# Kernel tuning notes

Measured on AMD Instinct MI355X. Metric: run time of the kernel, lower is better.

## Reference

```python
import jax, jax.numpy as jnp
import numpy as np

B, L, D = 4, 2048, 2048
H, KVH, HD = 16, 4, 128          # num_heads, num_kv_heads, head_dim = D // H
M = 16                           # mem_tokens
BASE = 10000.0
EPS = 1.1920929e-07              # torch F.rms_norm default eps = fp32 machine eps


def _rms_norm(x):
    # normalize over last dim, no learned weight (matches F.rms_norm(x, (hd,)))
    return x * jax.lax.rsqrt(jnp.mean(x * x, axis=-1, keepdims=True) + EPS)


def _apply_rotary(x, cos, sin):
    # x: [B, h, T, HD]; cos/sin: [1, 1, T, HD//2]
    half = x.shape[-1] // 2
    x1, x2 = x[..., :half], x[..., half:]
    return jnp.concatenate([x1 * cos + x2 * sin, -x1 * sin + x2 * cos], axis=-1)


def setup_inputs() -> dict:
    key = jax.random.key(0)
    k0, k1, k2, k3, k4 = jax.random.split(key, 5)
    kv_dim = KVH * HD
    s = 0.02
    return {
        "x": jax.random.normal(k0, (B, L, D), dtype=jnp.float32),
        "Wq": jax.random.normal(k1, (D, D), dtype=jnp.float32) * s,
        "Wk": jax.random.normal(k2, (kv_dim, D), dtype=jnp.float32) * s,
        "Wv": jax.random.normal(k3, (kv_dim, D), dtype=jnp.float32) * s,
        "Wproj": jax.random.normal(k4, (D, D), dtype=jnp.float32) * s,
        "q_gain": jnp.full((H,), 1.0, dtype=jnp.float32),
    }


def reference(x, Wq, Wk, Wv, Wproj, q_gain):
    Bx, Lx, Dx = x.shape
    # QKV projections (Linear: x @ W.T), split into heads -> [B, h, L, HD]
    q = (x @ Wq.T).reshape(Bx, Lx, H, HD).transpose(0, 2, 1, 3)
    k = (x @ Wk.T).reshape(Bx, Lx, KVH, HD).transpose(0, 2, 1, 3)
    v = (x @ Wv.T).reshape(Bx, Lx, KVH, HD).transpose(0, 2, 1, 3)
    # QK RMSNorm
    q = _rms_norm(q)
    k = _rms_norm(k)
    # RoPE on the non-memory tokens only
    T = Lx - M
    inv_freq = 1.0 / BASE ** (jnp.arange(0, HD, 2, dtype=jnp.float32) / HD)
    freqs = jnp.outer(jnp.arange(T, dtype=jnp.float32), inv_freq)  # [T, HD//2]
    cos = jnp.cos(freqs)[None, None]
    sin = jnp.sin(freqs)[None, None]
    q = jnp.concatenate([q[:, :, :M], _apply_rotary(q[:, :, M:], cos, sin)], axis=2)
    k = jnp.concatenate([k[:, :, :M], _apply_rotary(k[:, :, M:], cos, sin)], axis=2)
    # per-head gain on q
    q = q * q_gain[None, :, None, None]
    # GQA attention: group q heads by kv head (matches repeat_interleave ordering)
    rep = H // KVH
    qg = q.reshape(Bx, KVH, rep, Lx, HD)
    scale = 1.0 / np.sqrt(HD).astype(np.float32)
    scores = jnp.einsum('bgrqd,bgkd->bgrqk', qg, k) * scale  # [B, KVH, rep, L, L]
    causal = jnp.tril(jnp.ones((Lx, Lx), dtype=bool))
    scores = jnp.where(causal, scores, -jnp.inf)
    p = jax.nn.softmax(scores, axis=-1)
    y = jnp.einsum('bgrqk,bgkd->bgrqd', p, v)                # [B, KVH, rep, L, HD]
    y = y.reshape(Bx, H, Lx, HD).transpose(0, 2, 1, 3).reshape(Bx, Lx, Dx)
    return y @ Wproj.T
```

## Files before the change

kernel.cpp:

```cpp
#include <hip/hip_runtime.h>
#include <stdint.h>

typedef unsigned short u16;
typedef short s8v __attribute__((ext_vector_type(8)));
typedef float f4v __attribute__((ext_vector_type(4)));
typedef float f16v __attribute__((ext_vector_type(16)));

typedef __attribute__((address_space(1))) char gchar;
typedef __attribute__((address_space(3))) char lchar;

static __device__ __forceinline__ u16 f2bf(float f) {
  uint32_t x = __float_as_uint(f);
  x += 0x7fffu + ((x >> 16) & 1u);
  return (u16)(x >> 16);
}
static __device__ __forceinline__ float bf2f(u16 u) {
  return __uint_as_float(((uint32_t)u) << 16);
}
static __device__ __forceinline__ void gload_lds16(const void* g, void* l) {
  __builtin_amdgcn_global_load_lds((gchar*)(uintptr_t)g,
                                   (lchar*)(uint32_t)(uintptr_t)l, 16, 0, 0);
}

__global__ __launch_bounds__(256) void cvt_bf16(const float4* __restrict__ src,
                                                uint2* __restrict__ dst, int n4) {
  int i = blockIdx.x * 256 + threadIdx.x;
  int st = gridDim.x * 256;
  for (; i < n4; i += st) {
    float4 v = src[i];
    uint2 o;
    o.x = (uint32_t)f2bf(v.x) | ((uint32_t)f2bf(v.y) << 16);
    o.y = (uint32_t)f2bf(v.z) | ((uint32_t)f2bf(v.w) << 16);
    dst[i] = o;
  }
}

__global__ __launch_bounds__(256) void rope_table(float* __restrict__ tc,
                                                  float* __restrict__ ts) {
  int i = blockIdx.x * 256 + threadIdx.x;
  if (i >= 2032 * 64) return;
  int t = i >> 6, f = i & 63;
  float invf = 1.0f / powf(10000.0f, (float)f * (1.0f / 64.0f));
  float ang = (float)t * invf;
  float s, c;
  sincosf(ang, &s, &c);
  tc[i] = c;
  ts[i] = s;
}

template <int MODE>
__global__ __launch_bounds__(512, 2) void gemm_nt(
    const u16* __restrict__ A, const u16* __restrict__ W0,
    const u16* __restrict__ W1, const u16* __restrict__ W2,
    u16* __restrict__ O0, u16* __restrict__ O1, u16* __restrict__ O2,
    float* __restrict__ OF) {
  __shared__ u16 lA[3][256 * 32];
  __shared__ u16 lB[3][256 * 32];
  const int tid = threadIdx.x;
  const int lane = tid & 63, wid = tid >> 6;
  const int wr = wid >> 2, wc = wid & 3;
  const int l15 = lane & 15, l4 = lane >> 4;

  const int NB = (MODE == 0) ? 12 : 8;
  const int nwg = gridDim.x;
  const int bid = blockIdx.x;
  const int swz = (bid & 7) * (nwg >> 3) + (bid >> 3);
  const int bm = swz / NB, bn = swz % NB;
  const int m0 = bm * 256;

  const u16* Wt;
  int n0r;
  if constexpr (MODE == 0) {
    if (bn < 8)       { Wt = W0; n0r = bn * 256; }
    else if (bn < 10) { Wt = W1; n0r = (bn - 8) * 256; }
    else              { Wt = W2; n0r = (bn - 10) * 256; }
  } else {
    Wt = W0; n0r = bn * 256;
  }

  auto stage = [&](int kt, int bsel) {
    const int kb = kt * 32;
#pragma unroll
    for (int c = 0; c < 2; ++c) {
      int cidx = tid + c * 512;
      int p = cidx >> 3, q = cidx & 7;
      int qp = q ^ (p & 7);
      int r = 2 * p + (qp >> 2), k8 = qp & 3;
      gload_lds16(A + (size_t)(m0 + r) * 2048 + kb + k8 * 8, &lA[bsel][cidx * 8]);
    }
#pragma unroll
    for (int c = 0; c < 2; ++c) {
      int cidx = tid + c * 512;
      int p = cidx >> 3, q = cidx & 7;
      int qp = q ^ (p & 7);
      int r = 2 * p + (qp >> 2), k8 = qp & 3;
      gload_lds16(Wt + (size_t)(n0r + r) * 2048 + kb + k8 * 8, &lB[bsel][cidx * 8]);
    }
  };
  auto swzoff = [&](int fr, int s) {
    return (fr >> 1) * 64 + (((s + ((fr & 1) << 2)) ^ ((fr >> 1) & 7)) << 3);
  };

  const f4v Z4 = {0.f, 0.f, 0.f, 0.f};
  f4v acc[8][4];
#pragma unroll
  for (int i = 0; i < 8; i++)
#pragma unroll
    for (int j = 0; j < 4; j++) acc[i][j] = Z4;

  stage(0, 0);
  stage(1, 1);

  const int NT = 64;
  int cur = 0;
  for (int t = 0; t < NT; ++t) {
    asm volatile("s_waitcnt lgkmcnt(0)" ::: "memory");
    __builtin_amdgcn_sched_barrier(0);
    asm volatile("s_barrier" ::: "memory");
    const int nx2 = (cur == 0) ? 2 : cur - 1;
    if (t + 2 < NT) {
      stage(t + 2, nx2);
      asm volatile("s_waitcnt vmcnt(8)" ::: "memory");
    } else if (t + 1 < NT) {
      asm volatile("s_waitcnt vmcnt(4)" ::: "memory");
    } else {
      asm volatile("s_waitcnt vmcnt(0)" ::: "memory");
    }
    asm volatile("s_barrier" ::: "memory");

    const u16* pa = &lA[cur][0];
    const u16* pb = &lB[cur][0];
    s8v bfrg[4], afrg[4];
#pragma unroll
    for (int j = 0; j < 4; ++j)
      bfrg[j] = *(const s8v*)&pb[swzoff(wc * 64 + j * 16 + l15, l4)];
#pragma unroll
    for (int i = 0; i < 4; ++i)
      afrg[i] = *(const s8v*)&pa[swzoff(wr * 128 + i * 16 + l15, l4)];
    __builtin_amdgcn_s_setprio(1);
#pragma unroll
    for (int i = 0; i < 4; ++i)
#pragma unroll
      for (int j = 0; j < 4; ++j)
        acc[i][j] = __builtin_amdgcn_mfma_f32_16x16x32_bf16(afrg[i], bfrg[j], acc[i][j], 0, 0, 0);
    __builtin_amdgcn_s_setprio(0);
    asm volatile("s_barrier" ::: "memory");
#pragma unroll
    for (int i = 0; i < 4; ++i)
      afrg[i] = *(const s8v*)&pa[swzoff(wr * 128 + (i + 4) * 16 + l15, l4)];
    __builtin_amdgcn_s_setprio(1);
#pragma unroll
    for (int i = 0; i < 4; ++i)
#pragma unroll
      for (int j = 0; j < 4; ++j)
        acc[i + 4][j] = __builtin_amdgcn_mfma_f32_16x16x32_bf16(afrg[i], bfrg[j], acc[i + 4][j], 0, 0, 0);
    __builtin_amdgcn_s_setprio(0);

    cur = (cur == 2) ? 0 : cur + 1;
  }

  const int ncol0 = bn * 256 + wc * 64;
  if constexpr (MODE == 0) {
    u16* Ob; int hh, HX;
    if (ncol0 < 2048)      { Ob = O0; hh = ncol0 >> 7;          HX = 16; }
    else if (ncol0 < 2560) { Ob = O1; hh = (ncol0 - 2048) >> 7; HX = 4; }
    else                   { Ob = O2; hh = (ncol0 - 2560) >> 7; HX = 4; }
    const int d0 = ncol0 & 127;
#pragma unroll
    for (int i = 0; i < 8; i++)
#pragma unroll
      for (int r = 0; r < 4; r++) {
        int m = m0 + wr * 128 + i * 16 + l4 * 4 + r;
        int b = m >> 11, l = m & 2047;
        size_t base = ((size_t)(b * HX + hh) * 2048 + l) * 128 + d0;
#pragma unroll
        for (int j = 0; j < 4; j++)
          Ob[base + j * 16 + l15] = f2bf(acc[i][j][r]);
      }
  } else {
#pragma unroll
    for (int i = 0; i < 8; i++)
#pragma unroll
      for (int r = 0; r < 4; r++) {
        int m = m0 + wr * 128 + i * 16 + l4 * 4 + r;
#pragma unroll
        for (int j = 0; j < 4; j++)
          OF[(size_t)m * 2048 + ncol0 + j * 16 + l15] = acc[i][j][r];
      }
  }
}

__global__ __launch_bounds__(256) void norm_rope(u16* __restrict__ buf, int nh,
                                                 const float* __restrict__ gain,
                                                 const float* __restrict__ tc,
                                                 const float* __restrict__ ts,
                                                 int nrows) {
  const int lane = threadIdx.x & 63;
  const int gw = blockIdx.x * 4 + (threadIdx.x >> 6);
  const int nw = gridDim.x * 4;
  for (int row = gw; row < nrows; row += nw) {
    int l = row & 2047;
    int h = (row >> 11) % nh;
    u16* p = buf + (size_t)row * 128;
    float x1 = bf2f(p[lane]);
    float x2 = bf2f(p[lane + 64]);
    float ss = x1 * x1 + x2 * x2;
#pragma unroll
    for (int off = 32; off > 0; off >>= 1) ss += __shfl_xor(ss, off, 64);
    float r = rsqrtf(ss * (1.0f / 128.0f) + 1.1920929e-07f);
    x1 *= r; x2 *= r;
    if (l >= 16) {
      int t = l - 16;
      float c = tc[t * 64 + lane], s = ts[t * 64 + lane];
      float o1 = x1 * c + x2 * s;
      float o2 = -x1 * s + x2 * c;
      x1 = o1; x2 = o2;
    }
    if (gain) { float g = gain[h]; x1 *= g; x2 *= g; }
    p[lane] = f2bf(x1);
    p[lane + 64] = f2bf(x2);
  }
}

__global__ __launch_bounds__(256) void transpose_v(const u16* __restrict__ v,
                                                   u16* __restrict__ vt) {
  __shared__ u16 t[64][64];
  const int l0 = blockIdx.x * 64, d0 = blockIdx.y * 64, bg = blockIdx.z;
  const int tid = threadIdx.x;
#pragma unroll
  for (int it = 0; it < 2; ++it) {
    int lin = it * 256 + tid;
    int r = lin >> 3, cb = lin & 7;
    s8v val = *(const s8v*)&v[((bg * 2048 + l0 + r) * 128) + d0 + cb * 8];
    *(s8v*)&t[r][(cb ^ (r & 7)) * 8] = val;
  }
  __syncthreads();
#pragma unroll
  for (int it = 0; it < 2; ++it) {
    int lin = it * 256 + tid;
    int r2 = lin >> 3, c2 = (lin & 7) * 8;
    s8v o;
#pragma unroll
    for (int j = 0; j < 8; ++j) {
      int rr = c2 + j, cc = r2;
      o[j] = (short)t[rr][(cc & 7) + 8 * ((cc >> 3) ^ (rr & 7))];
    }
    *(s8v*)&vt[((bg * 128 + d0 + r2) * 2048) + l0 + c2] = o;
  }
}

__global__ __launch_bounds__(256, 2) void attn(const u16* __restrict__ q,
                                               const u16* __restrict__ k,
                                               const u16* __restrict__ vt,
                                               u16* __restrict__ y) {
  __shared__ u16 lK[2][64 * 128];
  __shared__ u16 lVT[2][128 * 64];
  const int tid = threadIdx.x;
  const int lane = tid & 63, wid = tid >> 6;
  const int l31 = lane & 31, hi = lane >> 5;

  const int db = (int)blockIdx.y * 32 + (int)blockIdx.x;
  const int half = db >> 8, rem = db & 255;
  const int bg = (rem & 7) + 8 * half;
  const int pairi = rem >> 3;
  const int b = bg >> 2, g = bg & 3;
  const int h = g * 4 + wid;

  const u16* qh = q + (size_t)(b * 16 + h) * 2048 * 128;
  const u16* kb0 = k + (size_t)(b * 4 + g) * 2048 * 128;
  const u16* vtb0 = vt + (size_t)(b * 4 + g) * 128 * 2048;
  const float scale = 0.08838834764831845f;

  auto stage = [&](int t, int bufsel) {
    const int kv0 = t * 64;
#pragma unroll
    for (int it = 0; it < 4; ++it) {
      int lin = it * 256 + tid;
      int kj = lin >> 4, s = lin & 15;
      gload_lds16(kb0 + (size_t)(kv0 + kj) * 128 + ((s ^ (kj & 7)) * 8),
                  &lK[bufsel][lin * 8]);
    }
#pragma unroll
    for (int it = 0; it < 4; ++it) {
      int lin = it * 256 + tid;
      int d = lin >> 3, s = lin & 7;
      gload_lds16(vtb0 + (size_t)d * 2048 + kv0 + ((s ^ (d & 7)) * 8),
                  &lVT[bufsel][lin * 8]);
    }
  };

  for (int ph = 0; ph < 2; ++ph) {
    const int qt = ph ? (63 - pairi) : pairi;
    const int q0 = qt * 32;
    const int nt = (q0 >> 6) + 1;
    const int qabs = q0 + l31;

    s8v qf[8];
#pragma unroll
    for (int ks = 0; ks < 8; ++ks)
      qf[ks] = *(const s8v*)&qh[(q0 + l31) * 128 + ks * 16 + hi * 8];

    f16v yacc[4];
#pragma unroll
    for (int j = 0; j < 4; ++j)
#pragma unroll
      for (int r = 0; r < 16; ++r) yacc[j][r] = 0.f;
    float mrow = -1e30f, lrow = 0.f;

    stage(0, 0);
    __syncthreads();

    for (int t = 0; t < nt; ++t) {
      const int cur = t & 1;
      if (t + 1 < nt) stage(t + 1, cur ^ 1);
      const int kv0 = t * 64;

      f16v s0a, s1a;
#pragma unroll
      for (int r = 0; r < 16; ++r) { s0a[r] = 0.f; s1a[r] = 0.f; }
#pragma unroll
      for (int ks = 0; ks < 8; ++ks) {
        const int slot = (2 * ks + hi) ^ (l31 & 7);
        s8v kf0 = *(const s8v*)&lK[cur][(l31)*128 + slot * 8];
        s8v kf1 = *(const s8v*)&lK[cur][(32 + l31) * 128 + slot * 8];
        s0a = __builtin_amdgcn_mfma_f32_32x32x16_bf16(kf0, qf[ks], s0a, 0, 0, 0);
        s1a = __builtin_amdgcn_mfma_f32_32x32x16_bf16(kf1, qf[ks], s1a, 0, 0, 0);
      }

      const bool last = (t == nt - 1);
      float p0[16], p1[16];
      float pmax = -1e30f;
#pragma unroll
      for (int r = 0; r < 16; ++r) {
        const int kvloc = (r & 3) + 8 * (r >> 2) + 4 * hi;
        float v0 = s0a[r] * scale;
        float v1 = s1a[r] * scale;
        if (last) {
          if (kv0 + kvloc > qabs) v0 = -1e30f;
          if (kv0 + 32 + kvloc > qabs) v1 = -1e30f;
        }
        p0[r] = v0; p1[r] = v1;
        pmax = fmaxf(pmax, fmaxf(v0, v1));
      }
      pmax = fmaxf(pmax, __shfl_xor(pmax, 32, 64));

      if (!__all(pmax - mrow <= 8.0f)) {
        float mnew = fmaxf(mrow, pmax);
        float corr = __expf(mrow - mnew);
#pragma unroll
        for (int r = 0; r < 16; ++r) {
          const int qloc = (r & 3) + 8 * (r >> 2) + 4 * hi;
          float cb = __shfl(corr, qloc, 64);
          yacc[0][r] *= cb; yacc[1][r] *= cb; yacc[2][r] *= cb; yacc[3][r] *= cb;
        }
        lrow *= corr;
        mrow = mnew;
      }

      float ps = 0.f;
#pragma unroll
      for (int r = 0; r < 16; ++r) {
        float e0 = bf2f(f2bf(__expf(p0[r] - mrow)));
        float e1 = bf2f(f2bf(__expf(p1[r] - mrow)));
        p0[r] = e0; p1[r] = e1;
        ps += e0 + e1;
      }
      ps += __shfl_xor(ps, 32, 64);
      lrow += ps;

#pragma unroll
      for (int ks = 0; ks < 4; ++ks) {
        const float* pc = (ks < 2) ? p0 : p1;
        const int rb = 8 * (ks & 1);
        uint32_t A0 = (uint32_t)f2bf(pc[rb + 0]) | ((uint32_t)f2bf(pc[rb + 1]) << 16);
        uint32_t A1 = (uint32_t)f2bf(pc[rb + 2]) | ((uint32_t)f2bf(pc[rb + 3]) << 16);
        uint32_t B0 = (uint32_t)f2bf(pc[rb + 4]) | ((uint32_t)f2bf(pc[rb + 5]) << 16);
        uint32_t B1 = (uint32_t)f2bf(pc[rb + 6]) | ((uint32_t)f2bf(pc[rb + 7]) << 16);
        uint32_t t0 = hi ? A0 : B0;
        uint32_t t1 = hi ? A1 : B1;
        uint32_t r0 = (uint32_t)__shfl_xor((int)t0, 32, 64);
        uint32_t r1 = (uint32_t)__shfl_xor((int)t1, 32, 64);
        union { uint32_t u[4]; s8v v; } uu;
        uu.u[0] = hi ? r0 : A0;
        uu.u[1] = hi ? r1 : A1;
        uu.u[2] = hi ? B0 : r0;
        uu.u[3] = hi ? B1 : r1;
#pragma unroll
        for (int jd = 0; jd < 4; ++jd) {
          const int rowd = 32 * jd + l31;
          const int slot = (2 * ks + hi) ^ (l31 & 7);
          s8v vf = *(const s8v*)&lVT[cur][rowd * 64 + slot * 8];
          yacc[jd] = __builtin_amdgcn_mfma_f32_32x32x16_bf16(uu.v, vf, yacc[jd], 0, 0, 0);
        }
      }
      __syncthreads();
    }

    float inv = 1.0f / lrow;
#pragma unroll
    for (int r = 0; r < 16; ++r) {
      const int qloc = (r & 3) + 8 * (r >> 2) + 4 * hi;
      float ib = __shfl(inv, qloc, 64);
      const int qrow = q0 + qloc;
      size_t base = ((size_t)(b * 2048 + qrow)) * 2048 + h * 128 + l31;
#pragma unroll
      for (int jd = 0; jd < 4; ++jd)
        y[base + 32 * jd] = f2bf(yacc[jd][r] * ib);
    }
  }
}

extern "C" void kernel_launch(void* const* d_in, const int* in_sizes, int n_in,
                              void* d_out, int out_size, void* d_ws, size_t ws_size,
                              hipStream_t stream) {
  const float* x  = (const float*)d_in[0];
  const float* Wq = (const float*)d_in[1];
  const float* Wk = (const float*)d_in[2];
  const float* Wv = (const float*)d_in[3];
  const float* Wp = (const float*)d_in[4];
  const float* qg = (const float*)d_in[5];
  float* out = (float*)d_out;

  char* ws = (char*)d_ws;
  size_t off = 0;
  auto alloc = [&](size_t bytes) {
    void* p = ws + off;
    off += (bytes + 255) & ~(size_t)255;
    return p;
  };
  u16* x_bf  = (u16*)alloc((size_t)8192 * 2048 * 2);
  u16* wq_bf = (u16*)alloc((size_t)2048 * 2048 * 2);
  u16* wk_bf = (u16*)alloc((size_t)512 * 2048 * 2);
  u16* wv_bf = (u16*)alloc((size_t)512 * 2048 * 2);
  u16* wp_bf = (u16*)alloc((size_t)2048 * 2048 * 2);
  u16* q_bf  = (u16*)alloc((size_t)4 * 16 * 2048 * 128 * 2);
  u16* k_bf  = (u16*)alloc((size_t)4 * 4 * 2048 * 128 * 2);
  u16* v_bf  = (u16*)alloc((size_t)4 * 4 * 2048 * 128 * 2);
  float* tab = (float*)alloc((size_t)2032 * 64 * 2 * 4);
  u16* y_bf  = x_bf;
  u16* vt_bf = wq_bf;

  cvt_bf16<<<2048, 256, 0, stream>>>((const float4*)x,  (uint2*)x_bf,  8192 * 2048 / 4);
  cvt_bf16<<<512,  256, 0, stream>>>((const float4*)Wq, (uint2*)wq_bf, 2048 * 2048 / 4);
  cvt_bf16<<<128,  256, 0, stream>>>((const float4*)Wk, (uint2*)wk_bf, 512 * 2048 / 4);
  cvt_bf16<<<128,  256, 0, stream>>>((const float4*)Wv, (uint2*)wv_bf, 512 * 2048 / 4);
  cvt_bf16<<<512,  256, 0, stream>>>((const float4*)Wp, (uint2*)wp_bf, 2048 * 2048 / 4);
  rope_table<<<(2032 * 64 + 255) / 256, 256, 0, stream>>>(tab, tab + 2032 * 64);

  gemm_nt<0><<<dim3(384), 512, 0, stream>>>(x_bf, wq_bf, wk_bf, wv_bf,
                                            q_bf, k_bf, v_bf, nullptr);
  norm_rope<<<2048, 256, 0, stream>>>(q_bf, 16, qg, tab, tab + 2032 * 64, 4 * 16 * 2048);
  norm_rope<<<512,  256, 0, stream>>>(k_bf, 4, nullptr, tab, tab + 2032 * 64, 4 * 4 * 2048);
  transpose_v<<<dim3(32, 2, 16), 256, 0, stream>>>(v_bf, vt_bf);
  attn<<<dim3(32, 16), 256, 0, stream>>>(q_bf, k_bf, vt_bf, y_bf);
  gemm_nt<1><<<dim3(256), 512, 0, stream>>>(y_bf, wp_bf, nullptr, nullptr,
                                            nullptr, nullptr, nullptr, out);
}
```

Before: 400.4 us.

## Shrink GEMM tile to 256x128 with 4-stage pipeline, merge conversion and norm launches

The GEMM tile changes from 256x256 to 256x128, the grid doubles and the LDS ring buffer goes from 3 to 4 stages with deeper prefetch. The four weight conversions merge into one kernel, and the q and k norm_rope launches merge into one, which relies on q and k being contiguous in the workspace. Attention MFMA sections get raised wave priority. The smaller tile gives more blocks but less operand reuse per block, and the merged kernels depend on the buffer layout staying contiguous.

```diff
diff --git a/kernel.cpp b/kernel.cpp
--- a/kernel.cpp
+++ b/kernel.cpp
@@ -28,6 +28,28 @@
   int st = gridDim.x * 256;
   for (; i < n4; i += st) {
     float4 v = src[i];
+    uint2 o;
+    o.x = (uint32_t)f2bf(v.x) | ((uint32_t)f2bf(v.y) << 16);
+    o.y = (uint32_t)f2bf(v.z) | ((uint32_t)f2bf(v.w) << 16);
+    dst[i] = o;
+  }
+}
+
+__global__ __launch_bounds__(256) void cvt_bf16_w(const float4* __restrict__ s0,
+                                                  const float4* __restrict__ s1,
+                                                  const float4* __restrict__ s2,
+                                                  const float4* __restrict__ s3,
+                                                  uint2* __restrict__ dst) {
+  int i = blockIdx.x * 256 + threadIdx.x;
+  int st = gridDim.x * 256;
+  for (; i < 2621440; i += st) {
+    const float4* s;
+    int off;
+    if (i < 1048576)      { s = s0; off = i; }
+    else if (i < 1310720) { s = s1; off = i - 1048576; }
+    else if (i < 1572864) { s = s2; off = i - 1310720; }
+    else                  { s = s3; off = i - 1572864; }
+    float4 v = s[off];
     uint2 o;
     o.x = (uint32_t)f2bf(v.x) | ((uint32_t)f2bf(v.y) << 16);
     o.y = (uint32_t)f2bf(v.z) | ((uint32_t)f2bf(v.w) << 16);
@@ -54,14 +76,14 @@
     const u16* __restrict__ W1, const u16* __restrict__ W2,
     u16* __restrict__ O0, u16* __restrict__ O1, u16* __restrict__ O2,
     float* __restrict__ OF) {
-  __shared__ u16 lA[3][256 * 32];
-  __shared__ u16 lB[3][256 * 32];
+  __shared__ u16 lA[4][256 * 32];
+  __shared__ u16 lB[4][128 * 32];
   const int tid = threadIdx.x;
   const int lane = tid & 63, wid = tid >> 6;
-  const int wr = wid >> 2, wc = wid & 3;
+  const int wr = wid >> 1, wc = wid & 1;
   const int l15 = lane & 15, l4 = lane >> 4;
 
-  const int NB = (MODE == 0) ? 12 : 8;
+  const int NB = (MODE == 0) ? 24 : 16;
   const int nwg = gridDim.x;
   const int bid = blockIdx.x;
   const int swz = (bid & 7) * (nwg >> 3) + (bid >> 3);
@@ -71,11 +93,11 @@
   const u16* Wt;
   int n0r;
   if constexpr (MODE == 0) {
-    if (bn < 8)       { Wt = W0; n0r = bn * 256; }
-    else if (bn < 10) { Wt = W1; n0r = (bn - 8) * 256; }
-    else              { Wt = W2; n0r = (bn - 10) * 256; }
+    if (bn < 16)      { Wt = W0; n0r = bn * 128; }
+    else if (bn < 20) { Wt = W1; n0r = (bn - 16) * 128; }
+    else              { Wt = W2; n0r = (bn - 20) * 128; }
   } else {
-    Wt = W0; n0r = bn * 256;
+    Wt = W0; n0r = bn * 128;
   }
 
   auto stage = [&](int kt, int bsel) {
@@ -88,9 +110,8 @@
       int r = 2 * p + (qp >> 2), k8 = qp & 3;
       gload_lds16(A + (size_t)(m0 + r) * 2048 + kb + k8 * 8, &lA[bsel][cidx * 8]);
     }
-#pragma unroll
-    for (int c = 0; c < 2; ++c) {
-      int cidx = tid + c * 512;
+    {
+      int cidx = tid;
       int p = cidx >> 3, q = cidx & 7;
       int qp = q ^ (p & 7);
       int r = 2 * p + (qp >> 2), k8 = qp & 3;
@@ -102,27 +123,29 @@
   };
 
   const f4v Z4 = {0.f, 0.f, 0.f, 0.f};
-  f4v acc[8][4];
-#pragma unroll
-  for (int i = 0; i < 8; i++)
+  f4v acc[4][4];
+#pragma unroll
+  for (int i = 0; i < 4; i++)
 #pragma unroll
     for (int j = 0; j < 4; j++) acc[i][j] = Z4;
 
   stage(0, 0);
   stage(1, 1);
+  stage(2, 2);
 
   const int NT = 64;
-  int cur = 0;
   for (int t = 0; t < NT; ++t) {
+    const int cur = t & 3;
     asm volatile("s_waitcnt lgkmcnt(0)" ::: "memory");
     __builtin_amdgcn_sched_barrier(0);
     asm volatile("s_barrier" ::: "memory");
-    const int nx2 = (cur == 0) ? 2 : cur - 1;
-    if (t + 2 < NT) {
-      stage(t + 2, nx2);
-      asm volatile("s_waitcnt vmcnt(8)" ::: "memory");
-    } else if (t + 1 < NT) {
-      asm volatile("s_waitcnt vmcnt(4)" ::: "memory");
+    if (t + 3 < NT) {
+      stage(t + 3, (t + 3) & 3);
+      asm volatile("s_waitcnt vmcnt(9)" ::: "memory");
+    } else if (t == NT - 3) {
+      asm volatile("s_waitcnt vmcnt(6)" ::: "memory");
+    } else if (t == NT - 2) {
+      asm volatile("s_waitcnt vmcnt(3)" ::: "memory");
     } else {
       asm volatile("s_waitcnt vmcnt(0)" ::: "memory");
     }
@@ -130,13 +153,13 @@
 
     const u16* pa = &lA[cur][0];
     const u16* pb = &lB[cur][0];
-    s8v bfrg[4], afrg[4];
+    s8v afrg[4], bfrg[4];
+#pragma unroll
+    for (int i = 0; i < 4; ++i)
+      afrg[i] = *(const s8v*)&pa[swzoff(wr * 64 + i * 16 + l15, l4)];
 #pragma unroll
     for (int j = 0; j < 4; ++j)
       bfrg[j] = *(const s8v*)&pb[swzoff(wc * 64 + j * 16 + l15, l4)];
-#pragma unroll
-    for (int i = 0; i < 4; ++i)
-      afrg[i] = *(const s8v*)&pa[swzoff(wr * 128 + i * 16 + l15, l4)];
     __builtin_amdgcn_s_setprio(1);
 #pragma unroll
     for (int i = 0; i < 4; ++i)
@@ -144,33 +167,21 @@
       for (int j = 0; j < 4; ++j)
         acc[i][j] = __builtin_amdgcn_mfma_f32_16x16x32_bf16(afrg[i], bfrg[j], acc[i][j], 0, 0, 0);
     __builtin_amdgcn_s_setprio(0);
-    asm volatile("s_barrier" ::: "memory");
-#pragma unroll
-    for (int i = 0; i < 4; ++i)
-      afrg[i] = *(const s8v*)&pa[swzoff(wr * 128 + (i + 4) * 16 + l15, l4)];
-    __builtin_amdgcn_s_setprio(1);
-#pragma unroll
-    for (int i = 0; i < 4; ++i)
-#pragma unroll
-      for (int j = 0; j < 4; ++j)
-        acc[i + 4][j] = __builtin_amdgcn_mfma_f32_16x16x32_bf16(afrg[i], bfrg[j], acc[i + 4][j], 0, 0, 0);
-    __builtin_amdgcn_s_setprio(0);
-
-    cur = (cur == 2) ? 0 : cur + 1;
-  }
-
-  const int ncol0 = bn * 256 + wc * 64;
+  }
+
+  const int ncol0 = bn * 128 + wc * 64;
   if constexpr (MODE == 0) {
+    const int colg = ncol0;
     u16* Ob; int hh, HX;
-    if (ncol0 < 2048)      { Ob = O0; hh = ncol0 >> 7;          HX = 16; }
-    else if (ncol0 < 2560) { Ob = O1; hh = (ncol0 - 2048) >> 7; HX = 4; }
-    else                   { Ob = O2; hh = (ncol0 - 2560) >> 7; HX = 4; }
-    const int d0 = ncol0 & 127;
-#pragma unroll
-    for (int i = 0; i < 8; i++)
+    if (colg < 2048)      { Ob = O0; hh = colg >> 7;          HX = 16; }
+    else if (colg < 2560) { Ob = O1; hh = (colg - 2048) >> 7; HX = 4; }
+    else                  { Ob = O2; hh = (colg - 2560) >> 7; HX = 4; }
+    const int d0 = colg & 127;
+#pragma unroll
+    for (int i = 0; i < 4; i++)
 #pragma unroll
       for (int r = 0; r < 4; r++) {
-        int m = m0 + wr * 128 + i * 16 + l4 * 4 + r;
+        int m = m0 + wr * 64 + i * 16 + l4 * 4 + r;
         int b = m >> 11, l = m & 2047;
         size_t base = ((size_t)(b * HX + hh) * 2048 + l) * 128 + d0;
 #pragma unroll
@@ -179,10 +190,10 @@
       }
   } else {
 #pragma unroll
-    for (int i = 0; i < 8; i++)
+    for (int i = 0; i < 4; i++)
 #pragma unroll
       for (int r = 0; r < 4; r++) {
-        int m = m0 + wr * 128 + i * 16 + l4 * 4 + r;
+        int m = m0 + wr * 64 + i * 16 + l4 * 4 + r;
 #pragma unroll
         for (int j = 0; j < 4; j++)
           OF[(size_t)m * 2048 + ncol0 + j * 16 + l15] = acc[i][j][r];
@@ -190,17 +201,15 @@
   }
 }
 
-__global__ __launch_bounds__(256) void norm_rope(u16* __restrict__ buf, int nh,
+__global__ __launch_bounds__(256) void norm_rope(u16* __restrict__ buf,
                                                  const float* __restrict__ gain,
                                                  const float* __restrict__ tc,
-                                                 const float* __restrict__ ts,
-                                                 int nrows) {
+                                                 const float* __restrict__ ts) {
   const int lane = threadIdx.x & 63;
   const int gw = blockIdx.x * 4 + (threadIdx.x >> 6);
   const int nw = gridDim.x * 4;
-  for (int row = gw; row < nrows; row += nw) {
+  for (int row = gw; row < 163840; row += nw) {
     int l = row & 2047;
-    int h = (row >> 11) % nh;
     u16* p = buf + (size_t)row * 128;
     float x1 = bf2f(p[lane]);
     float x2 = bf2f(p[lane + 64]);
@@ -216,7 +225,10 @@
       float o2 = -x1 * s + x2 * c;
       x1 = o1; x2 = o2;
     }
-    if (gain) { float g = gain[h]; x1 *= g; x2 *= g; }
+    if (row < 131072) {
+      float g = gain[(row >> 11) & 15];
+      x1 *= g; x2 *= g;
+    }
     p[lane] = f2bf(x1);
     p[lane + 64] = f2bf(x2);
   }
@@ -318,6 +330,7 @@
       f16v s0a, s1a;
 #pragma unroll
       for (int r = 0; r < 16; ++r) { s0a[r] = 0.f; s1a[r] = 0.f; }
+      __builtin_amdgcn_s_setprio(1);
 #pragma unroll
       for (int ks = 0; ks < 8; ++ks) {
         const int slot = (2 * ks + hi) ^ (l31 & 7);
@@ -326,6 +339,7 @@
         s0a = __builtin_amdgcn_mfma_f32_32x32x16_bf16(kf0, qf[ks], s0a, 0, 0, 0);
         s1a = __builtin_amdgcn_mfma_f32_32x32x16_bf16(kf1, qf[ks], s1a, 0, 0, 0);
       }
+      __builtin_amdgcn_s_setprio(0);
 
       const bool last = (t == nt - 1);
       float p0[16], p1[16];
@@ -368,6 +382,7 @@
       ps += __shfl_xor(ps, 32, 64);
       lrow += ps;
 
+      __builtin_amdgcn_s_setprio(1);
 #pragma unroll
       for (int ks = 0; ks < 4; ++ks) {
         const float* pc = (ks < 2) ? p0 : p1;
@@ -393,6 +408,7 @@
           yacc[jd] = __builtin_amdgcn_mfma_f32_32x32x16_bf16(uu.v, vf, yacc[jd], 0, 0, 0);
         }
       }
+      __builtin_amdgcn_s_setprio(0);
       __syncthreads();
     }
 
@@ -440,19 +456,17 @@
   u16* y_bf  = x_bf;
   u16* vt_bf = wq_bf;
 
-  cvt_bf16<<<2048, 256, 0, stream>>>((const float4*)x,  (uint2*)x_bf,  8192 * 2048 / 4);
-  cvt_bf16<<<512,  256, 0, stream>>>((const float4*)Wq, (uint2*)wq_bf, 2048 * 2048 / 4);
-  cvt_bf16<<<128,  256, 0, stream>>>((const float4*)Wk, (uint2*)wk_bf, 512 * 2048 / 4);
-  cvt_bf16<<<128,  256, 0, stream>>>((const float4*)Wv, (uint2*)wv_bf, 512 * 2048 / 4);
-  cvt_bf16<<<512,  256, 0, stream>>>((const float4*)Wp, (uint2*)wp_bf, 2048 * 2048 / 4);
+  cvt_bf16<<<2048, 256, 0, stream>>>((const float4*)x, (uint2*)x_bf, 8192 * 2048 / 4);
+  cvt_bf16_w<<<1024, 256, 0, stream>>>((const float4*)Wq, (const float4*)Wk,
+                                       (const float4*)Wv, (const float4*)Wp,
+                                       (uint2*)wq_bf);
   rope_table<<<(2032 * 64 + 255) / 256, 256, 0, stream>>>(tab, tab + 2032 * 64);
 
-  gemm_nt<0><<<dim3(384), 512, 0, stream>>>(x_bf, wq_bf, wk_bf, wv_bf,
+  gemm_nt<0><<<dim3(768), 512, 0, stream>>>(x_bf, wq_bf, wk_bf, wv_bf,
                                             q_bf, k_bf, v_bf, nullptr);
-  norm_rope<<<2048, 256, 0, stream>>>(q_bf, 16, qg, tab, tab + 2032 * 64, 4 * 16 * 2048);
-  norm_rope<<<512,  256, 0, stream>>>(k_bf, 4, nullptr, tab, tab + 2032 * 64, 4 * 4 * 2048);
+  norm_rope<<<2048, 256, 0, stream>>>(q_bf, qg, tab, tab + 2032 * 64);
   transpose_v<<<dim3(32, 2, 16), 256, 0, stream>>>(v_bf, vt_bf);
   attn<<<dim3(32, 16), 256, 0, stream>>>(q_bf, k_bf, vt_bf, y_bf);
-  gemm_nt<1><<<dim3(256), 512, 0, stream>>>(y_bf, wp_bf, nullptr, nullptr,
+  gemm_nt<1><<<dim3(512), 512, 0, stream>>>(y_bf, wp_bf, nullptr, nullptr,
                                             nullptr, nullptr, nullptr, out);
 }
```

Measured after the change: 376.3 us. 6.0% less time.
